# Kernel tuning notes

Hardware: AMD Instinct MI355X
Metric: run time of the kernel (lower is better)

## Reference

```python
import jax, jax.numpy as jnp
import numpy as np

IN_F, OUT_F, RANK = 4096, 4096, 16
SCALING = 1.0  # alpha defaults to rank -> alpha/rank == 1.0


def setup_inputs() -> dict:
    key = jax.random.key(0)
    k1, k2, k3, k4 = jax.random.split(key, 4)
    x = jax.random.normal(k1, (4, 2048, IN_F), dtype=jnp.float32)
    base_weight = jax.random.normal(k2, (OUT_F, IN_F), dtype=jnp.float32)
    U = jax.random.normal(k3, (OUT_F, RANK), dtype=jnp.float32)
    s = jnp.ones((RANK,), dtype=jnp.float32)
    V = jax.random.normal(k4, (IN_F, RANK), dtype=jnp.float32)
    return {"x": x, "base_weight": base_weight, "U": U, "s": s, "V": V}


def reference(x, base_weight, U, s, V):
    # delta_weight = scaling * (U * s) @ V^T, shape (out, in)
    delta_w = SCALING * jnp.einsum('or,ir->oi', U * s[None, :], V)
    adapted = base_weight + delta_w
    # x @ adapted^T : (..., in) -> (..., out)
    return jnp.einsum('bsi,oi->bso', x, adapted)
```

## Files before the change

kernel.cpp:

```cpp
#include <hip/hip_runtime.h>


#define IN_F   4096
#define OUT_F  4096
#define RANK   16
#define M_ROWS 8192
#define BM 256
#define BN 256
#define BK 64
#define NT (IN_F / BK)

typedef _Float16 f16x8 __attribute__((ext_vector_type(8)));
typedef _Float16 f16x4 __attribute__((ext_vector_type(4)));
typedef float    f32x4 __attribute__((ext_vector_type(4)));

__device__ __forceinline__ void async16(const void* gp, void* lp) {
  __builtin_amdgcn_global_load_lds(
      (const __attribute__((address_space(1))) void*)gp,
      (__attribute__((address_space(3))) void*)lp, 16, 0, 0);
}

#define SPLIT_BLOCKS 4096

__global__ __launch_bounds__(256)
void prep_kernel(const float* __restrict__ x, _Float16* __restrict__ xh,
                 const float* __restrict__ W, const float* __restrict__ U,
                 const float* __restrict__ S, const float* __restrict__ V,
                 _Float16* __restrict__ wh) {
  if (blockIdx.x < SPLIT_BLOCKS) {
    size_t t = (size_t)blockIdx.x * 256 + threadIdx.x;
#pragma unroll
    for (int it = 0; it < 8; ++it) {
      float4 v = ((const float4*)x)[t];
      f16x4 h;
      h[0] = (_Float16)v.x; h[1] = (_Float16)v.y;
      h[2] = (_Float16)v.z; h[3] = (_Float16)v.w;
      ((f16x4*)xh)[t] = h;
      t += (size_t)SPLIT_BLOCKS * 256;
    }
  } else {
    int t = (int)(blockIdx.x - SPLIT_BLOCKS) * 256 + threadIdx.x;
    int i4 = (t & 1023) << 2;
    int o0 = (t >> 10) << 3;

    float v[4][RANK];
#pragma unroll
    for (int j = 0; j < 4; ++j) {
      const float4* vp = (const float4*)(V + (size_t)(i4 + j) * RANK);
#pragma unroll
      for (int q = 0; q < 4; ++q) {
        float4 vv = vp[q];
        v[j][q * 4 + 0] = vv.x; v[j][q * 4 + 1] = vv.y;
        v[j][q * 4 + 2] = vv.z; v[j][q * 4 + 3] = vv.w;
      }
    }
    float sv[RANK];
#pragma unroll
    for (int r = 0; r < RANK; r += 4) {
      float4 ss = *(const float4*)(S + r);
      sv[r] = ss.x; sv[r + 1] = ss.y; sv[r + 2] = ss.z; sv[r + 3] = ss.w;
    }

    for (int oo = 0; oo < 8; ++oo) {
      int o = o0 + oo;
      float us[RANK];
      const float4* up = (const float4*)(U + (size_t)o * RANK);
#pragma unroll
      for (int r = 0; r < RANK; r += 4) {
        float4 uu = up[r >> 2];
        us[r] = uu.x * sv[r]; us[r + 1] = uu.y * sv[r + 1];
        us[r + 2] = uu.z * sv[r + 2]; us[r + 3] = uu.w * sv[r + 3];
      }
      float4 w = *(const float4*)(W + (size_t)o * IN_F + i4);
      float d0 = w.x, d1 = w.y, d2 = w.z, d3 = w.w;
#pragma unroll
      for (int r = 0; r < RANK; ++r) {
        d0 += us[r] * v[0][r];
        d1 += us[r] * v[1][r];
        d2 += us[r] * v[2][r];
        d3 += us[r] * v[3][r];
      }
      f16x4 h;
      h[0] = (_Float16)d0; h[1] = (_Float16)d1;
      h[2] = (_Float16)d2; h[3] = (_Float16)d3;
      *(f16x4*)(wh + (size_t)o * IN_F + i4) = h;
    }
  }
}

__global__ __launch_bounds__(512, 2)
void gemm_kernel(const _Float16* __restrict__ xh,
                 const _Float16* __restrict__ wh,
                 float* __restrict__ out) {
  __shared__ unsigned char lds[131072];

  const int orig = blockIdx.x;
  const int wg = (orig & 7) * 64 + (orig >> 3);
  const int mt = wg >> 4;
  const int nt = wg & 15;
  const int blockM = mt * BM;
  const int blockN = nt * BN;

  const int tid = threadIdx.x;
  const int lane = tid & 63;
  const int wave = tid >> 6;
  const int wm = wave >> 2;
  const int wn = wave & 3;

  const _Float16* aSrc[2];
  const _Float16* bSrc[2];
  unsigned ldsOff[2];
#pragma unroll
  for (int q = 0; q < 2; ++q) {
    int slot = q * 512 + tid;
    int r = slot >> 2;
    int c = slot & 3;
    int cd = c ^ ((r >> 1) & 3);
    aSrc[q] = xh + (size_t)(blockM + r) * IN_F + cd * 8;
    bSrc[q] = wh + (size_t)(blockN + r) * IN_F + cd * 8;
    ldsOff[q] = (unsigned)slot * 16;
  }

  const int kg = lane >> 4;
  unsigned offA[4], offB[4];
#pragma unroll
  for (int t = 0; t < 4; ++t) {
    int ar = wm * 128 + t * 16 + (lane & 15);
    offA[t] = (unsigned)(ar * 64 + ((kg ^ ((ar >> 1) & 3)) * 16));
    int br = wn * 64 + t * 16 + (lane & 15);
    offB[t] = (unsigned)(br * 64 + ((kg ^ ((br >> 1) & 3)) * 16));
  }

  f32x4 acc[8][4];
#pragma unroll
  for (int i = 0; i < 8; ++i)
#pragma unroll
    for (int j = 0; j < 4; ++j) acc[i][j] = (f32x4){0.f, 0.f, 0.f, 0.f};

#define STG(SRC, LDSBASE, KOFS)                                      \
  {                                                                  \
    async16(SRC[0] + (KOFS), lds + (LDSBASE) + ldsOff[0]);           \
    async16(SRC[1] + (KOFS), lds + (LDSBASE) + ldsOff[1]);           \
  }

  STG(aSrc, 0, 0);
  STG(bSrc, 16384, 0);
  STG(aSrc, 32768, 32);
  STG(bSrc, 49152, 32);
  STG(bSrc, 65536 + 16384, 64);
  STG(aSrc, 65536 + 0, 64);
  STG(bSrc, 65536 + 49152, 96);
  asm volatile("s_waitcnt vmcnt(6)" ::: "memory");
  __builtin_amdgcn_s_barrier();

#pragma unroll 2
  for (int t = 0; t < NT; ++t) {
    const unsigned base = (unsigned)(t & 1) << 16;
    const unsigned baseN = base ^ 65536u;
    const int kof1 = (t + 1) * BK;
    const int kof2 = (t + 2) * BK;
    const bool ok1 = (t + 1) < NT;
    const bool ok2 = (t + 2) < NT;

    if (t >= NT - 2) {
      asm volatile("s_waitcnt vmcnt(0)" ::: "memory");
      __builtin_amdgcn_s_barrier();
    }

    f16x8 aF[4], bF[4];

#pragma unroll
    for (int i = 0; i < 4; ++i)
      aF[i] = *(const f16x8*)(lds + base + offA[i]);
#pragma unroll
    for (int j = 0; j < 4; ++j)
      bF[j] = *(const f16x8*)(lds + base + 16384 + offB[j]);
    if (ok1) STG(aSrc, baseN + 32768, kof1 + 32);
    __builtin_amdgcn_s_barrier();
    asm volatile("s_waitcnt lgkmcnt(0)" ::: "memory");
    __builtin_amdgcn_sched_barrier(0);
    __builtin_amdgcn_s_setprio(1);
#pragma unroll
    for (int i = 0; i < 4; ++i)
#pragma unroll
      for (int j = 0; j < 4; ++j)
        acc[i][j] = __builtin_amdgcn_mfma_f32_16x16x32_f16(aF[i], bF[j], acc[i][j], 0, 0, 0);
    __builtin_amdgcn_s_setprio(0);
    __builtin_amdgcn_s_barrier();

#pragma unroll
    for (int i = 0; i < 4; ++i)
      aF[i] = *(const f16x8*)(lds + base + 4096 + offA[i]);
    if (ok2) STG(bSrc, base + 16384, kof2);
    __builtin_amdgcn_s_barrier();
    asm volatile("s_waitcnt lgkmcnt(0)" ::: "memory");
    __builtin_amdgcn_sched_barrier(0);
    __builtin_amdgcn_s_setprio(1);
#pragma unroll
    for (int i = 0; i < 4; ++i)
#pragma unroll
      for (int j = 0; j < 4; ++j)
        acc[4 + i][j] = __builtin_amdgcn_mfma_f32_16x16x32_f16(aF[i], bF[j], acc[4 + i][j], 0, 0, 0);
    __builtin_amdgcn_s_setprio(0);
    __builtin_amdgcn_s_barrier();

#pragma unroll
    for (int i = 0; i < 4; ++i)
      aF[i] = *(const f16x8*)(lds + base + 32768 + offA[i]);
#pragma unroll
    for (int j = 0; j < 4; ++j)
      bF[j] = *(const f16x8*)(lds + base + 49152 + offB[j]);
    if (ok2) STG(aSrc, base + 0, kof2);
    __builtin_amdgcn_s_barrier();
    asm volatile("s_waitcnt lgkmcnt(0)" ::: "memory");
    __builtin_amdgcn_sched_barrier(0);
    __builtin_amdgcn_s_setprio(1);
#pragma unroll
    for (int i = 0; i < 4; ++i)
#pragma unroll
      for (int j = 0; j < 4; ++j)
        acc[i][j] = __builtin_amdgcn_mfma_f32_16x16x32_f16(aF[i], bF[j], acc[i][j], 0, 0, 0);
    __builtin_amdgcn_s_setprio(0);
    __builtin_amdgcn_s_barrier();

#pragma unroll
    for (int i = 0; i < 4; ++i)
      aF[i] = *(const f16x8*)(lds + base + 32768 + 4096 + offA[i]);
    if (ok2) STG(bSrc, base + 49152, kof2 + 32);
    asm volatile("s_waitcnt vmcnt(6)" ::: "memory");
    __builtin_amdgcn_s_barrier();
    asm volatile("s_waitcnt lgkmcnt(0)" ::: "memory");
    __builtin_amdgcn_sched_barrier(0);
    __builtin_amdgcn_s_setprio(1);
#pragma unroll
    for (int i = 0; i < 4; ++i)
#pragma unroll
      for (int j = 0; j < 4; ++j)
        acc[4 + i][j] = __builtin_amdgcn_mfma_f32_16x16x32_f16(aF[i], bF[j], acc[4 + i][j], 0, 0, 0);
    __builtin_amdgcn_s_setprio(0);
    __builtin_amdgcn_s_barrier();
  }
#undef STG

  const int col0 = blockN + wn * 64 + (lane & 15);
  const int row0 = blockM + wm * 128 + (lane >> 4) * 4;
#pragma unroll
  for (int i = 0; i < 8; ++i)
#pragma unroll
    for (int j = 0; j < 4; ++j) {
      float* op = out + (size_t)(row0 + i * 16) * OUT_F + col0 + j * 16;
#pragma unroll
      for (int rr = 0; rr < 4; ++rr) op[(size_t)rr * OUT_F] = acc[i][j][rr];
    }
}

__global__ __launch_bounds__(256)
void fb_gemm(const float* __restrict__ x, const float* __restrict__ W,
             float* __restrict__ out) {
  __shared__ float xs[64][17];
  __shared__ float wsm[64][17];
  const int mt = blockIdx.x >> 6;
  const int ntile = blockIdx.x & 63;
  const int bM = mt * 64, bN = ntile * 64;
  const int t = threadIdx.x;
  const int lr = t >> 2, lc = (t & 3) * 4;
  const int tm = t >> 4, tn = t & 15;

  float acc[4][4];
#pragma unroll
  for (int i = 0; i < 4; ++i)
#pragma unroll
    for (int j = 0; j < 4; ++j) acc[i][j] = 0.f;

  for (int kk = 0; kk < IN_F; kk += 16) {
    float4 xa = *(const float4*)(x + (size_t)(bM + lr) * IN_F + kk + lc);
    float4 wa = *(const float4*)(W + (size_t)(bN + lr) * IN_F + kk + lc);
    xs[lr][lc + 0] = xa.x; xs[lr][lc + 1] = xa.y;
    xs[lr][lc + 2] = xa.z; xs[lr][lc + 3] = xa.w;
    wsm[lr][lc + 0] = wa.x; wsm[lr][lc + 1] = wa.y;
    wsm[lr][lc + 2] = wa.z; wsm[lr][lc + 3] = wa.w;
    __syncthreads();
#pragma unroll
    for (int k = 0; k < 16; ++k) {
      float a[4], b[4];
#pragma unroll
      for (int i = 0; i < 4; ++i) a[i] = xs[tm * 4 + i][k];
#pragma unroll
      for (int j = 0; j < 4; ++j) b[j] = wsm[tn * 4 + j][k];
#pragma unroll
      for (int i = 0; i < 4; ++i)
#pragma unroll
        for (int j = 0; j < 4; ++j) acc[i][j] += a[i] * b[j];
    }
    __syncthreads();
  }
#pragma unroll
  for (int i = 0; i < 4; ++i)
#pragma unroll
    for (int j = 0; j < 4; ++j)
      out[(size_t)(bM + tm * 4 + i) * OUT_F + bN + tn * 4 + j] = acc[i][j];
}

__global__ void fb_xv(const float* __restrict__ x, const float* __restrict__ V,
                      const float* __restrict__ S, float* __restrict__ xv) {
  int m = blockIdx.x * 4 + (threadIdx.x >> 6);
  int lane = threadIdx.x & 63;
  float a[RANK];
#pragma unroll
  for (int r = 0; r < RANK; ++r) a[r] = 0.f;
  for (int k = lane; k < IN_F; k += 64) {
    float xe = x[(size_t)m * IN_F + k];
    const float4* vp = (const float4*)(V + (size_t)k * RANK);
#pragma unroll
    for (int q = 0; q < 4; ++q) {
      float4 vv = vp[q];
      a[q * 4 + 0] += xe * vv.x; a[q * 4 + 1] += xe * vv.y;
      a[q * 4 + 2] += xe * vv.z; a[q * 4 + 3] += xe * vv.w;
    }
  }
#pragma unroll
  for (int r = 0; r < RANK; ++r)
    for (int off = 32; off; off >>= 1) a[r] += __shfl_down(a[r], off);
  if (lane == 0) {
#pragma unroll
    for (int r = 0; r < RANK; ++r) xv[(size_t)m * RANK + r] = a[r] * S[r];
  }
}

__global__ void fb_add(const float* __restrict__ xv, const float* __restrict__ U,
                       float* __restrict__ out) {
  size_t t = (size_t)blockIdx.x * 256 + threadIdx.x;
  int m = (int)(t >> 12), o = (int)(t & 4095);
  const float* xr = xv + (size_t)m * RANK;
  const float* ur = U + (size_t)o * RANK;
  float d = 0.f;
#pragma unroll
  for (int r = 0; r < RANK; ++r) d += xr[r] * ur[r];
  out[t] += d;
}

extern "C" void kernel_launch(void* const* d_in, const int* in_sizes, int n_in,
                              void* d_out, int out_size, void* d_ws, size_t ws_size,
                              hipStream_t stream) {
  const float* x = (const float*)d_in[0];
  const float* W = (const float*)d_in[1];
  const float* U = (const float*)d_in[2];
  const float* s = (const float*)d_in[3];
  const float* V = (const float*)d_in[4];
  float* out = (float*)d_out;

  const size_t need = ((size_t)M_ROWS * IN_F + (size_t)OUT_F * IN_F) * 2;
  if (ws_size >= need) {
    _Float16* xh = (_Float16*)d_ws;
    _Float16* wh = xh + (size_t)M_ROWS * IN_F;
    prep_kernel<<<SPLIT_BLOCKS + ((IN_F / 4) * (OUT_F / 8)) / 256, 256, 0, stream>>>(
        x, xh, W, U, s, V, wh);
    gemm_kernel<<<(M_ROWS / BM) * (OUT_F / BN), 512, 0, stream>>>(xh, wh, out);
  } else {
    float* xv = (float*)d_ws;
    fb_gemm<<<(M_ROWS / 64) * (OUT_F / 64), 256, 0, stream>>>(x, W, out);
    fb_xv<<<M_ROWS / 4, 256, 0, stream>>>(x, V, s, xv);
    fb_add<<<(size_t)M_ROWS * OUT_F / 256, 256, 0, stream>>>(xv, U, out);
  }
}
```

Before: 545.5 us.

## Fuse fp32-to-fp16 conversion of x into GEMM loads via register staging

Removes the separate pass that converts x to fp16 in workspace. The GEMM now loads fp32 x tiles into registers with inline global loads, converts them, and writes them to LDS inside the pipelined loop, while W tiles keep using async global-to-LDS copies. This saves writing and re-reading a 64MB fp16 copy of x, but doubles the bytes read for the A operand on every tile reload, adds VGPR pressure and conversion ALU work, and makes the vmcnt wait accounting more complex.

```diff
diff --git a/kernel.cpp b/kernel.cpp
--- a/kernel.cpp
+++ b/kernel.cpp
@@ -20,76 +20,68 @@
       (__attribute__((address_space(3))) void*)lp, 16, 0, 0);
 }
 
-#define SPLIT_BLOCKS 4096
+__device__ __forceinline__ f32x4 gload(const float* p) {
+  f32x4 r;
+  asm volatile("global_load_dwordx4 %0, %1, off" : "=v"(r) : "v"(p));
+  return r;
+}
 
 __global__ __launch_bounds__(256)
-void prep_kernel(const float* __restrict__ x, _Float16* __restrict__ xh,
-                 const float* __restrict__ W, const float* __restrict__ U,
-                 const float* __restrict__ S, const float* __restrict__ V,
-                 _Float16* __restrict__ wh) {
-  if (blockIdx.x < SPLIT_BLOCKS) {
-    size_t t = (size_t)blockIdx.x * 256 + threadIdx.x;
-#pragma unroll
-    for (int it = 0; it < 8; ++it) {
-      float4 v = ((const float4*)x)[t];
-      f16x4 h;
-      h[0] = (_Float16)v.x; h[1] = (_Float16)v.y;
-      h[2] = (_Float16)v.z; h[3] = (_Float16)v.w;
-      ((f16x4*)xh)[t] = h;
-      t += (size_t)SPLIT_BLOCKS * 256;
-    }
-  } else {
-    int t = (int)(blockIdx.x - SPLIT_BLOCKS) * 256 + threadIdx.x;
-    int i4 = (t & 1023) << 2;
-    int o0 = (t >> 10) << 3;
-
-    float v[4][RANK];
-#pragma unroll
-    for (int j = 0; j < 4; ++j) {
-      const float4* vp = (const float4*)(V + (size_t)(i4 + j) * RANK);
-#pragma unroll
-      for (int q = 0; q < 4; ++q) {
-        float4 vv = vp[q];
-        v[j][q * 4 + 0] = vv.x; v[j][q * 4 + 1] = vv.y;
-        v[j][q * 4 + 2] = vv.z; v[j][q * 4 + 3] = vv.w;
-      }
-    }
-    float sv[RANK];
+void prep_w_kernel(const float* __restrict__ W,
+                   const float* __restrict__ U,
+                   const float* __restrict__ S,
+                   const float* __restrict__ V,
+                   _Float16* __restrict__ wh) {
+  int t = blockIdx.x * 256 + threadIdx.x;
+  int i4 = (t & 1023) << 2;
+  int o0 = (t >> 10) << 3;
+
+  float v[4][RANK];
+#pragma unroll
+  for (int j = 0; j < 4; ++j) {
+    const float4* vp = (const float4*)(V + (size_t)(i4 + j) * RANK);
+#pragma unroll
+    for (int q = 0; q < 4; ++q) {
+      float4 vv = vp[q];
+      v[j][q * 4 + 0] = vv.x; v[j][q * 4 + 1] = vv.y;
+      v[j][q * 4 + 2] = vv.z; v[j][q * 4 + 3] = vv.w;
+    }
+  }
+  float sv[RANK];
+#pragma unroll
+  for (int r = 0; r < RANK; r += 4) {
+    float4 ss = *(const float4*)(S + r);
+    sv[r] = ss.x; sv[r + 1] = ss.y; sv[r + 2] = ss.z; sv[r + 3] = ss.w;
+  }
+
+  for (int oo = 0; oo < 8; ++oo) {
+    int o = o0 + oo;
+    float us[RANK];
+    const float4* up = (const float4*)(U + (size_t)o * RANK);
 #pragma unroll
     for (int r = 0; r < RANK; r += 4) {
-      float4 ss = *(const float4*)(S + r);
-      sv[r] = ss.x; sv[r + 1] = ss.y; sv[r + 2] = ss.z; sv[r + 3] = ss.w;
-    }
-
-    for (int oo = 0; oo < 8; ++oo) {
-      int o = o0 + oo;
-      float us[RANK];
-      const float4* up = (const float4*)(U + (size_t)o * RANK);
-#pragma unroll
-      for (int r = 0; r < RANK; r += 4) {
-        float4 uu = up[r >> 2];
-        us[r] = uu.x * sv[r]; us[r + 1] = uu.y * sv[r + 1];
-        us[r + 2] = uu.z * sv[r + 2]; us[r + 3] = uu.w * sv[r + 3];
-      }
-      float4 w = *(const float4*)(W + (size_t)o * IN_F + i4);
-      float d0 = w.x, d1 = w.y, d2 = w.z, d3 = w.w;
-#pragma unroll
-      for (int r = 0; r < RANK; ++r) {
-        d0 += us[r] * v[0][r];
-        d1 += us[r] * v[1][r];
-        d2 += us[r] * v[2][r];
-        d3 += us[r] * v[3][r];
-      }
-      f16x4 h;
-      h[0] = (_Float16)d0; h[1] = (_Float16)d1;
-      h[2] = (_Float16)d2; h[3] = (_Float16)d3;
-      *(f16x4*)(wh + (size_t)o * IN_F + i4) = h;
-    }
+      float4 uu = up[r >> 2];
+      us[r] = uu.x * sv[r]; us[r + 1] = uu.y * sv[r + 1];
+      us[r + 2] = uu.z * sv[r + 2]; us[r + 3] = uu.w * sv[r + 3];
+    }
+    float4 w = *(const float4*)(W + (size_t)o * IN_F + i4);
+    float d0 = w.x, d1 = w.y, d2 = w.z, d3 = w.w;
+#pragma unroll
+    for (int r = 0; r < RANK; ++r) {
+      d0 += us[r] * v[0][r];
+      d1 += us[r] * v[1][r];
+      d2 += us[r] * v[2][r];
+      d3 += us[r] * v[3][r];
+    }
+    f16x4 h;
+    h[0] = (_Float16)d0; h[1] = (_Float16)d1;
+    h[2] = (_Float16)d2; h[3] = (_Float16)d3;
+    *(f16x4*)(wh + (size_t)o * IN_F + i4) = h;
   }
 }
 
 __global__ __launch_bounds__(512, 2)
-void gemm_kernel(const _Float16* __restrict__ xh,
+void gemm_kernel(const float* __restrict__ x,
                  const _Float16* __restrict__ wh,
                  float* __restrict__ out) {
   __shared__ unsigned char lds[131072];
@@ -107,18 +99,21 @@
   const int wm = wave >> 2;
   const int wn = wave & 3;
 
-  const _Float16* aSrc[2];
+  const float*    aSrc0;
+  const float*    aSrc1;
   const _Float16* bSrc[2];
-  unsigned ldsOff[2];
-#pragma unroll
-  for (int q = 0; q < 2; ++q) {
-    int slot = q * 512 + tid;
-    int r = slot >> 2;
-    int c = slot & 3;
-    int cd = c ^ ((r >> 1) & 3);
-    aSrc[q] = xh + (size_t)(blockM + r) * IN_F + cd * 8;
-    bSrc[q] = wh + (size_t)(blockN + r) * IN_F + cd * 8;
-    ldsOff[q] = (unsigned)slot * 16;
+  unsigned ldsOff0, ldsOff1;
+  {
+    int slot = tid;
+    int r = slot >> 2, c = slot & 3, cd = c ^ ((r >> 1) & 3);
+    aSrc0 = x + (size_t)(blockM + r) * IN_F + cd * 8;
+    bSrc[0] = wh + (size_t)(blockN + r) * IN_F + cd * 8;
+    ldsOff0 = (unsigned)slot * 16;
+    slot = tid + 512;
+    r = slot >> 2; c = slot & 3; cd = c ^ ((r >> 1) & 3);
+    aSrc1 = x + (size_t)(blockM + r) * IN_F + cd * 8;
+    bSrc[1] = wh + (size_t)(blockN + r) * IN_F + cd * 8;
+    ldsOff1 = (unsigned)slot * 16;
   }
 
   const int kg = lane >> 4;
@@ -137,36 +132,64 @@
 #pragma unroll
     for (int j = 0; j < 4; ++j) acc[i][j] = (f32x4){0.f, 0.f, 0.f, 0.f};
 
-#define STG(SRC, LDSBASE, KOFS)                                      \
+  f32x4 s0a = {0,0,0,0}, s0b = {0,0,0,0}, s0c = {0,0,0,0}, s0d = {0,0,0,0};
+  f32x4 s1a = {0,0,0,0}, s1b = {0,0,0,0}, s1c = {0,0,0,0}, s1d = {0,0,0,0};
+
+#define STG(LDSBASE, KOFS)                                           \
   {                                                                  \
-    async16(SRC[0] + (KOFS), lds + (LDSBASE) + ldsOff[0]);           \
-    async16(SRC[1] + (KOFS), lds + (LDSBASE) + ldsOff[1]);           \
-  }
-
-  STG(aSrc, 0, 0);
-  STG(bSrc, 16384, 0);
-  STG(aSrc, 32768, 32);
-  STG(bSrc, 49152, 32);
-  STG(bSrc, 65536 + 16384, 64);
-  STG(aSrc, 65536 + 0, 64);
-  STG(bSrc, 65536 + 49152, 96);
-  asm volatile("s_waitcnt vmcnt(6)" ::: "memory");
+    async16(bSrc[0] + (KOFS), lds + (LDSBASE) + ldsOff0);            \
+    async16(bSrc[1] + (KOFS), lds + (LDSBASE) + ldsOff1);            \
+  }
+
+#define CVTW(REGOFF, P, Q, R, S)                                     \
+  {                                                                  \
+    f16x8 h0, h1;                                                    \
+    h0[0] = (_Float16)(P)[0]; h0[1] = (_Float16)(P)[1];              \
+    h0[2] = (_Float16)(P)[2]; h0[3] = (_Float16)(P)[3];              \
+    h0[4] = (_Float16)(Q)[0]; h0[5] = (_Float16)(Q)[1];              \
+    h0[6] = (_Float16)(Q)[2]; h0[7] = (_Float16)(Q)[3];              \
+    h1[0] = (_Float16)(R)[0]; h1[1] = (_Float16)(R)[1];              \
+    h1[2] = (_Float16)(R)[2]; h1[3] = (_Float16)(R)[3];              \
+    h1[4] = (_Float16)(S)[0]; h1[5] = (_Float16)(S)[1];              \
+    h1[6] = (_Float16)(S)[2]; h1[7] = (_Float16)(S)[3];              \
+    *(f16x8*)(lds + (REGOFF) + ldsOff0) = h0;                        \
+    *(f16x8*)(lds + (REGOFF) + ldsOff1) = h1;                        \
+  }
+
+  {
+    f32x4 p0 = *(const f32x4*)(aSrc0 + 0);
+    f32x4 p1 = *(const f32x4*)(aSrc0 + 4);
+    f32x4 p2 = *(const f32x4*)(aSrc1 + 0);
+    f32x4 p3 = *(const f32x4*)(aSrc1 + 4);
+    f32x4 q0 = *(const f32x4*)(aSrc0 + 32);
+    f32x4 q1 = *(const f32x4*)(aSrc0 + 36);
+    f32x4 q2 = *(const f32x4*)(aSrc1 + 32);
+    f32x4 q3 = *(const f32x4*)(aSrc1 + 36);
+    CVTW(0,     p0, p1, p2, p3);
+    CVTW(32768, q0, q1, q2, q3);
+    asm volatile("s_waitcnt vmcnt(0)" ::: "memory");
+  }
+  STG(16384, 0);
+  STG(49152, 32);
+  STG(65536 + 16384, 64);
+  s1a = gload(aSrc0 + 64); s1b = gload(aSrc0 + 68);
+  s1c = gload(aSrc1 + 64); s1d = gload(aSrc1 + 68);
+  STG(65536 + 49152, 96);
+  asm volatile("s_waitcnt vmcnt(8)" ::: "memory");
+  asm volatile("s_waitcnt lgkmcnt(0)" ::: "memory");
   __builtin_amdgcn_s_barrier();
+
+  const float* aP0 = aSrc0;
+  const float* aP1 = aSrc1;
 
 #pragma unroll 2
   for (int t = 0; t < NT; ++t) {
     const unsigned base = (unsigned)(t & 1) << 16;
     const unsigned baseN = base ^ 65536u;
-    const int kof1 = (t + 1) * BK;
     const int kof2 = (t + 2) * BK;
     const bool ok1 = (t + 1) < NT;
     const bool ok2 = (t + 2) < NT;
 
-    if (t >= NT - 2) {
-      asm volatile("s_waitcnt vmcnt(0)" ::: "memory");
-      __builtin_amdgcn_s_barrier();
-    }
-
     f16x8 aF[4], bF[4];
 
 #pragma unroll
@@ -175,7 +198,10 @@
 #pragma unroll
     for (int j = 0; j < 4; ++j)
       bF[j] = *(const f16x8*)(lds + base + 16384 + offB[j]);
-    if (ok1) STG(aSrc, baseN + 32768, kof1 + 32);
+    if (ok1) {
+      s0a = gload(aP0 + 96);  s0b = gload(aP0 + 100);
+      s0c = gload(aP1 + 96);  s0d = gload(aP1 + 100);
+    }
     __builtin_amdgcn_s_barrier();
     asm volatile("s_waitcnt lgkmcnt(0)" ::: "memory");
     __builtin_amdgcn_sched_barrier(0);
@@ -191,7 +217,11 @@
 #pragma unroll
     for (int i = 0; i < 4; ++i)
       aF[i] = *(const f16x8*)(lds + base + 4096 + offA[i]);
-    if (ok2) STG(bSrc, base + 16384, kof2);
+    if (ok2) STG(base + 16384, kof2);
+    if (ok2) { asm volatile("s_waitcnt vmcnt(8)" ::: "memory"); }
+    else     { asm volatile("s_waitcnt vmcnt(0)" ::: "memory"); }
+    __builtin_amdgcn_sched_barrier(0);
+    if (ok1) CVTW(baseN + 0, s1a, s1b, s1c, s1d);
     __builtin_amdgcn_s_barrier();
     asm volatile("s_waitcnt lgkmcnt(0)" ::: "memory");
     __builtin_amdgcn_sched_barrier(0);
@@ -210,7 +240,10 @@
 #pragma unroll
     for (int j = 0; j < 4; ++j)
       bF[j] = *(const f16x8*)(lds + base + 49152 + offB[j]);
-    if (ok2) STG(aSrc, base + 0, kof2);
+    if (ok2) {
+      s1a = gload(aP0 + 128); s1b = gload(aP0 + 132);
+      s1c = gload(aP1 + 128); s1d = gload(aP1 + 132);
+    }
     __builtin_amdgcn_s_barrier();
     asm volatile("s_waitcnt lgkmcnt(0)" ::: "memory");
     __builtin_amdgcn_sched_barrier(0);
@@ -226,8 +259,11 @@
 #pragma unroll
     for (int i = 0; i < 4; ++i)
       aF[i] = *(const f16x8*)(lds + base + 32768 + 4096 + offA[i]);
-    if (ok2) STG(bSrc, base + 49152, kof2 + 32);
-    asm volatile("s_waitcnt vmcnt(6)" ::: "memory");
+    if (ok2) STG(base + 49152, kof2 + 32);
+    if (ok2) { asm volatile("s_waitcnt vmcnt(8)" ::: "memory"); }
+    else     { asm volatile("s_waitcnt vmcnt(0)" ::: "memory"); }
+    __builtin_amdgcn_sched_barrier(0);
+    if (ok1) CVTW(baseN + 32768, s0a, s0b, s0c, s0d);
     __builtin_amdgcn_s_barrier();
     asm volatile("s_waitcnt lgkmcnt(0)" ::: "memory");
     __builtin_amdgcn_sched_barrier(0);
@@ -239,8 +275,11 @@
         acc[4 + i][j] = __builtin_amdgcn_mfma_f32_16x16x32_f16(aF[i], bF[j], acc[4 + i][j], 0, 0, 0);
     __builtin_amdgcn_s_setprio(0);
     __builtin_amdgcn_s_barrier();
+
+    aP0 += BK; aP1 += BK;
   }
 #undef STG
+#undef CVTW
 
   const int col0 = blockN + wn * 64 + (lane & 15);
   const int row0 = blockM + wm * 128 + (lane >> 4) * 4;
@@ -349,13 +388,11 @@
   const float* V = (const float*)d_in[4];
   float* out = (float*)d_out;
 
-  const size_t need = ((size_t)M_ROWS * IN_F + (size_t)OUT_F * IN_F) * 2;
+  const size_t need = (size_t)OUT_F * IN_F * 2;
   if (ws_size >= need) {
-    _Float16* xh = (_Float16*)d_ws;
-    _Float16* wh = xh + (size_t)M_ROWS * IN_F;
-    prep_kernel<<<SPLIT_BLOCKS + ((IN_F / 4) * (OUT_F / 8)) / 256, 256, 0, stream>>>(
-        x, xh, W, U, s, V, wh);
-    gemm_kernel<<<(M_ROWS / BM) * (OUT_F / BN), 512, 0, stream>>>(xh, wh, out);
+    _Float16* wh = (_Float16*)d_ws;
+    prep_w_kernel<<<((IN_F / 4) * (OUT_F / 8)) / 256, 256, 0, stream>>>(W, U, s, V, wh);
+    gemm_kernel<<<(M_ROWS / BM) * (OUT_F / BN), 512, 0, stream>>>(x, wh, out);
   } else {
     float* xv = (float*)d_ws;
     fb_gemm<<<(M_ROWS / 64) * (OUT_F / 64), 256, 0, stream>>>(x, W, out);
```

Result: slower. 559.9 us (+2.6%).

## Software-pipeline LDS fragment reads one phase ahead with double register buffers

Applied to the files above, without the earlier changes.

Restructures the main GEMM K-loop so that LDS fragment reads for the next MFMA phase are issued before the current phase's MFMAs. Two register buffer sets are used, and partial lgkmcnt waits replace full drains, so LDS read latency overlaps with MFMA execution. The last two iterations are peeled into an explicit epilogue, which removes the per-iteration bounds checks. Barriers drop from two per phase to one. This raises register pressure from the extra fragment buffers and depends on hand-counted waitcnt values being correct.

```diff
diff --git a/kernel.cpp b/kernel.cpp
--- a/kernel.cpp
+++ b/kernel.cpp
@@ -137,10 +137,35 @@
 #pragma unroll
     for (int j = 0; j < 4; ++j) acc[i][j] = (f32x4){0.f, 0.f, 0.f, 0.f};
 
+  f16x8 aFA[4], aFB[4], bF0[4], bF1[4];
+
 #define STG(SRC, LDSBASE, KOFS)                                      \
   {                                                                  \
     async16(SRC[0] + (KOFS), lds + (LDSBASE) + ldsOff[0]);           \
     async16(SRC[1] + (KOFS), lds + (LDSBASE) + ldsOff[1]);           \
+  }
+#define RD4(DST, RB, OFF)                                            \
+  {                                                                  \
+    DST[0] = *(const f16x8*)(lds + (RB) + OFF[0]);                   \
+    DST[1] = *(const f16x8*)(lds + (RB) + OFF[1]);                   \
+    DST[2] = *(const f16x8*)(lds + (RB) + OFF[2]);                   \
+    DST[3] = *(const f16x8*)(lds + (RB) + OFF[3]);                   \
+  }
+#define PH_BAR() asm volatile("s_barrier" ::: "memory")
+#define WAITL(N) asm volatile("s_waitcnt lgkmcnt(" #N ")" ::: "memory")
+#define WAITV(N) asm volatile("s_waitcnt vmcnt(" #N ")" ::: "memory")
+#define MFMA16(AO, A, B)                                             \
+  {                                                                  \
+    __builtin_amdgcn_sched_barrier(0);                               \
+    __builtin_amdgcn_s_setprio(1);                                   \
+    _Pragma("unroll")                                                \
+    for (int i_ = 0; i_ < 4; ++i_) {                                 \
+      _Pragma("unroll")                                              \
+      for (int j_ = 0; j_ < 4; ++j_)                                 \
+        acc[(AO) + i_][j_] = __builtin_amdgcn_mfma_f32_16x16x32_f16( \
+            (A)[i_], (B)[j_], acc[(AO) + i_][j_], 0, 0, 0);          \
+    }                                                                \
+    __builtin_amdgcn_s_setprio(0);                                   \
   }
 
   STG(aSrc, 0, 0);
@@ -150,97 +175,101 @@
   STG(bSrc, 65536 + 16384, 64);
   STG(aSrc, 65536 + 0, 64);
   STG(bSrc, 65536 + 49152, 96);
-  asm volatile("s_waitcnt vmcnt(6)" ::: "memory");
-  __builtin_amdgcn_s_barrier();
+  WAITV(6);
+  PH_BAR();
+  RD4(aFA, 0, offA);
+  RD4(bF0, 16384, offB);
 
 #pragma unroll 2
-  for (int t = 0; t < NT; ++t) {
-    const unsigned base = (unsigned)(t & 1) << 16;
+  for (int t = 0; t < NT - 2; ++t) {
+    const unsigned base  = (unsigned)(t & 1) << 16;
     const unsigned baseN = base ^ 65536u;
     const int kof1 = (t + 1) * BK;
     const int kof2 = (t + 2) * BK;
-    const bool ok1 = (t + 1) < NT;
-    const bool ok2 = (t + 2) < NT;
-
-    if (t >= NT - 2) {
-      asm volatile("s_waitcnt vmcnt(0)" ::: "memory");
-      __builtin_amdgcn_s_barrier();
-    }
-
-    f16x8 aF[4], bF[4];
-
-#pragma unroll
-    for (int i = 0; i < 4; ++i)
-      aF[i] = *(const f16x8*)(lds + base + offA[i]);
-#pragma unroll
-    for (int j = 0; j < 4; ++j)
-      bF[j] = *(const f16x8*)(lds + base + 16384 + offB[j]);
-    if (ok1) STG(aSrc, baseN + 32768, kof1 + 32);
-    __builtin_amdgcn_s_barrier();
-    asm volatile("s_waitcnt lgkmcnt(0)" ::: "memory");
-    __builtin_amdgcn_sched_barrier(0);
-    __builtin_amdgcn_s_setprio(1);
-#pragma unroll
-    for (int i = 0; i < 4; ++i)
-#pragma unroll
-      for (int j = 0; j < 4; ++j)
-        acc[i][j] = __builtin_amdgcn_mfma_f32_16x16x32_f16(aF[i], bF[j], acc[i][j], 0, 0, 0);
-    __builtin_amdgcn_s_setprio(0);
-    __builtin_amdgcn_s_barrier();
-
-#pragma unroll
-    for (int i = 0; i < 4; ++i)
-      aF[i] = *(const f16x8*)(lds + base + 4096 + offA[i]);
-    if (ok2) STG(bSrc, base + 16384, kof2);
-    __builtin_amdgcn_s_barrier();
-    asm volatile("s_waitcnt lgkmcnt(0)" ::: "memory");
-    __builtin_amdgcn_sched_barrier(0);
-    __builtin_amdgcn_s_setprio(1);
-#pragma unroll
-    for (int i = 0; i < 4; ++i)
-#pragma unroll
-      for (int j = 0; j < 4; ++j)
-        acc[4 + i][j] = __builtin_amdgcn_mfma_f32_16x16x32_f16(aF[i], bF[j], acc[4 + i][j], 0, 0, 0);
-    __builtin_amdgcn_s_setprio(0);
-    __builtin_amdgcn_s_barrier();
-
-#pragma unroll
-    for (int i = 0; i < 4; ++i)
-      aF[i] = *(const f16x8*)(lds + base + 32768 + offA[i]);
-#pragma unroll
-    for (int j = 0; j < 4; ++j)
-      bF[j] = *(const f16x8*)(lds + base + 49152 + offB[j]);
-    if (ok2) STG(aSrc, base + 0, kof2);
-    __builtin_amdgcn_s_barrier();
-    asm volatile("s_waitcnt lgkmcnt(0)" ::: "memory");
-    __builtin_amdgcn_sched_barrier(0);
-    __builtin_amdgcn_s_setprio(1);
-#pragma unroll
-    for (int i = 0; i < 4; ++i)
-#pragma unroll
-      for (int j = 0; j < 4; ++j)
-        acc[i][j] = __builtin_amdgcn_mfma_f32_16x16x32_f16(aF[i], bF[j], acc[i][j], 0, 0, 0);
-    __builtin_amdgcn_s_setprio(0);
-    __builtin_amdgcn_s_barrier();
-
-#pragma unroll
-    for (int i = 0; i < 4; ++i)
-      aF[i] = *(const f16x8*)(lds + base + 32768 + 4096 + offA[i]);
-    if (ok2) STG(bSrc, base + 49152, kof2 + 32);
-    asm volatile("s_waitcnt vmcnt(6)" ::: "memory");
-    __builtin_amdgcn_s_barrier();
-    asm volatile("s_waitcnt lgkmcnt(0)" ::: "memory");
-    __builtin_amdgcn_sched_barrier(0);
-    __builtin_amdgcn_s_setprio(1);
-#pragma unroll
-    for (int i = 0; i < 4; ++i)
-#pragma unroll
-      for (int j = 0; j < 4; ++j)
-        acc[4 + i][j] = __builtin_amdgcn_mfma_f32_16x16x32_f16(aF[i], bF[j], acc[4 + i][j], 0, 0, 0);
-    __builtin_amdgcn_s_setprio(0);
-    __builtin_amdgcn_s_barrier();
+
+    PH_BAR();
+    RD4(aFB, base + 4096, offA);
+    STG(aSrc, baseN + 32768, kof1 + 32);
+    WAITL(4);
+    MFMA16(0, aFA, bF0);
+
+    PH_BAR();
+    RD4(aFA, base + 32768, offA);
+    RD4(bF1, base + 49152, offB);
+    STG(bSrc, base + 16384, kof2);
+    WAITL(8);
+    MFMA16(4, aFB, bF0);
+
+    PH_BAR();
+    RD4(aFB, base + 32768 + 4096, offA);
+    STG(aSrc, base + 0, kof2);
+    WAITL(4);
+    MFMA16(0, aFA, bF1);
+
+    WAITV(4);
+    PH_BAR();
+    RD4(aFA, baseN + 0, offA);
+    RD4(bF0, baseN + 16384, offB);
+    STG(bSrc, base + 49152, kof2 + 32);
+    WAITL(8);
+    MFMA16(4, aFB, bF1);
+  }
+
+  {
+    const unsigned base = 0, baseN = 65536u;
+    const int kof1 = (NT - 1) * BK;
+    PH_BAR();
+    RD4(aFB, base + 4096, offA);
+    STG(aSrc, baseN + 32768, kof1 + 32);
+    WAITL(4);
+    MFMA16(0, aFA, bF0);
+
+    PH_BAR();
+    RD4(aFA, base + 32768, offA);
+    RD4(bF1, base + 49152, offB);
+    WAITL(8);
+    MFMA16(4, aFB, bF0);
+
+    PH_BAR();
+    RD4(aFB, base + 32768 + 4096, offA);
+    WAITL(4);
+    MFMA16(0, aFA, bF1);
+
+    WAITV(0);
+    PH_BAR();
+    RD4(aFA, baseN + 0, offA);
+    RD4(bF0, baseN + 16384, offB);
+    WAITL(8);
+    MFMA16(4, aFB, bF1);
+  }
+  {
+    const unsigned base = 65536u;
+    PH_BAR();
+    RD4(aFB, base + 4096, offA);
+    WAITL(4);
+    MFMA16(0, aFA, bF0);
+
+    PH_BAR();
+    RD4(aFA, base + 32768, offA);
+    RD4(bF1, base + 49152, offB);
+    WAITL(8);
+    MFMA16(4, aFB, bF0);
+
+    PH_BAR();
+    RD4(aFB, base + 32768 + 4096, offA);
+    WAITL(4);
+    MFMA16(0, aFA, bF1);
+
+    PH_BAR();
+    WAITL(0);
+    MFMA16(4, aFB, bF1);
   }
 #undef STG
+#undef RD4
+#undef PH_BAR
+#undef WAITL
+#undef WAITV
+#undef MFMA16
 
   const int col0 = blockN + wn * 64 + (lane & 15);
   const int row0 = blockM + wm * 128 + (lane >> 4) * 4;
```

After: 537.9 us. About the same (-1.4%).
